# Performance work log

Measured on AMD Instinct MI355X. Metric: run time of the kernel, lower is better.

The kernel has to match this reference:

```python
import jax, jax.numpy as jnp
import numpy as np

N_QUBITS = 8
N_LAYERS = 4
BATCH = 4096


def _ry(theta):
    # RY(theta) = [[cos(t/2), -sin(t/2)], [sin(t/2), cos(t/2)]]
    c = jnp.cos(theta / 2).astype(jnp.complex64)
    s = jnp.sin(theta / 2).astype(jnp.complex64)
    return jnp.stack([jnp.stack([c, -s], axis=-1),
                      jnp.stack([s, c], axis=-1)], axis=-2)  # (..., 2, 2)


def _rz(theta):
    # RZ(theta) = diag(exp(-i t/2), exp(+i t/2))
    p = jnp.exp(-0.5j * theta.astype(jnp.complex64))
    z = jnp.zeros_like(p)
    return jnp.stack([jnp.stack([p, z], axis=-1),
                      jnp.stack([z, jnp.conj(p)], axis=-1)], axis=-2)


def _apply_1q(state, U, w):
    # state: (B, 2, 2, ..., 2); apply 2x2 unitary U on wire w (axis 1+w).
    st = jnp.moveaxis(state, 1 + w, -1)
    if U.ndim == 3:  # per-sample (batched) gate, U: (B, 2, 2)
        st = jnp.einsum('bij,b...j->b...i', U, st)
    else:            # shared gate, U: (2, 2)
        st = jnp.einsum('ij,b...j->b...i', U, st)
    return jnp.moveaxis(st, -1, 1 + w)


def _apply_cnot(state, c, t):
    # flip target wire t where control wire c is |1>
    st = jnp.moveaxis(state, (1 + c, 1 + t), (-2, -1))
    st = jnp.concatenate([st[..., 0:1, :], st[..., 1:2, ::-1]], axis=-2)
    return jnp.moveaxis(st, (-2, -1), (1 + c, 1 + t))


def _circuit(x, weights):
    B = x.shape[0]
    state = jnp.zeros((B,) + (2,) * N_QUBITS, jnp.complex64)
    state = state.at[(slice(None),) + (0,) * N_QUBITS].set(1.0)  # |0...0>
    # Angle encoding: RY(x_i) on each wire, batched over samples
    for i in range(N_QUBITS):
        state = _apply_1q(state, _ry(x[:, i]), i)
    # Variational layers: CNOT ring then RY/RZ rotations
    for l in range(N_LAYERS):
        for i in range(N_QUBITS):
            state = _apply_cnot(state, i, (i + 1) % N_QUBITS)
        for i in range(N_QUBITS):
            state = _apply_1q(state, _ry(weights[l, i, 0]), i)
            state = _apply_1q(state, _rz(weights[l, i, 1]), i)
    # <Z_0> = P(q0=0) - P(q0=1)
    probs = jnp.sum(jnp.abs(state.reshape(B, 2, -1)) ** 2, axis=-1)
    return (probs[:, 0] - probs[:, 1]).astype(jnp.float32)


def setup_inputs() -> dict:
    key = jax.random.key(0)
    k1, k2 = jax.random.split(key)
    x = jax.random.uniform(k1, (BATCH, N_QUBITS), dtype=jnp.float32) * jnp.pi
    weights = jax.random.normal(k2, (N_LAYERS, N_QUBITS, 2), dtype=jnp.float32) * 0.1
    return {"x": x, "weights": weights}


def reference(x, weights):
    return _circuit(x, weights)
```

## Files before the change

kernel.cpp:

```cpp
#include <hip/hip_runtime.h>

#define NQ 8
#define NL 4
#define BATCH 4096


template <int CTRL>
__device__ __forceinline__ float dppx(float v) {
  return __int_as_float(
      __builtin_amdgcn_update_dpp(0, __float_as_int(v), CTRL, 0xF, 0xF, true));
}

__device__ __forceinline__ float swz4(float v) {
  return __int_as_float(
      __builtin_amdgcn_ds_swizzle(__float_as_int(v), 0x101F));
}

template <int W>
__device__ __forceinline__ float xl(float v) {
  if constexpr (W == 0) return dppx<0x128>(v);
  else if constexpr (W == 1) return swz4(v);
  else if constexpr (W == 2) return dppx<0x4E>(v);
  else return dppx<0xB1>(v);
}

template <int W>
__device__ __forceinline__ void ry_gate(float re[16], float im[16],
                                        float c, float s, int lane) {
  if constexpr (W <= 3) {
    const float ss = ((lane >> (3 - W)) & 1) ? s : -s;
#pragma unroll
    for (int r = 0; r < 16; ++r) {
      float pr = xl<W>(re[r]);
      float pi = xl<W>(im[r]);
      re[r] = c * re[r] + ss * pr;
      im[r] = c * im[r] + ss * pi;
    }
  } else {
    constexpr int m = 1 << (7 - W);
#pragma unroll
    for (int r = 0; r < 16; ++r) {
      if ((r & m) == 0) {
        const int r1 = r | m;
        float a0r = re[r], a1r = re[r1];
        float a0i = im[r], a1i = im[r1];
        re[r]  = c * a0r - s * a1r;
        re[r1] = s * a0r + c * a1r;
        im[r]  = c * a0i - s * a1i;
        im[r1] = s * a0i + c * a1i;
      }
    }
  }
}

template <int W>
__device__ __forceinline__ void rz_gate(float re[16], float im[16],
                                        float c, float s, int lane) {
  if constexpr (W <= 3) {
    const float ss = ((lane >> (3 - W)) & 1) ? s : -s;
#pragma unroll
    for (int r = 0; r < 16; ++r) {
      float nr = re[r] * c - im[r] * ss;
      float ni = im[r] * c + re[r] * ss;
      re[r] = nr; im[r] = ni;
    }
  } else {
    constexpr int m = 1 << (7 - W);
#pragma unroll
    for (int r = 0; r < 16; ++r) {
      const float ss = (r & m) ? s : -s;
      float nr = re[r] * c - im[r] * ss;
      float ni = im[r] * c + re[r] * ss;
      re[r] = nr; im[r] = ni;
    }
  }
}

__device__ __forceinline__ void cnot_ring(float re[16], float im[16], int lane) {
  {
    const bool p = (lane & 8) != 0;
#pragma unroll
    for (int r = 0; r < 16; ++r) {
      float pr = swz4(re[r]), pi = swz4(im[r]);
      re[r] = p ? pr : re[r];
      im[r] = p ? pi : im[r];
    }
  }
  {
    const bool p = (lane & 4) != 0;
#pragma unroll
    for (int r = 0; r < 16; ++r) {
      float pr = dppx<0x4E>(re[r]), pi = dppx<0x4E>(im[r]);
      re[r] = p ? pr : re[r];
      im[r] = p ? pi : im[r];
    }
  }
  {
    const bool p = (lane & 2) != 0;
#pragma unroll
    for (int r = 0; r < 16; ++r) {
      float pr = dppx<0xB1>(re[r]), pi = dppx<0xB1>(im[r]);
      re[r] = p ? pr : re[r];
      im[r] = p ? pi : im[r];
    }
  }
  {
    const bool p = (lane & 1) != 0;
#pragma unroll
    for (int r = 0; r < 8; ++r) {
      float t0r = re[r], t1r = re[r + 8];
      re[r] = p ? t1r : t0r; re[r + 8] = p ? t0r : t1r;
      float t0i = im[r], t1i = im[r + 8];
      im[r] = p ? t1i : t0i; im[r + 8] = p ? t0i : t1i;
    }
  }
#pragma unroll
  for (int r = 8; r < 12; ++r) {
    float t = re[r]; re[r] = re[r + 4]; re[r + 4] = t;
    t = im[r]; im[r] = im[r + 4]; im[r + 4] = t;
  }
#pragma unroll
  for (int r = 0; r < 16; ++r) {
    if ((r & 4) && !(r & 2)) {
      float t = re[r]; re[r] = re[r | 2]; re[r | 2] = t;
      t = im[r]; im[r] = im[r | 2]; im[r | 2] = t;
    }
  }
#pragma unroll
  for (int r = 0; r < 16; ++r) {
    if ((r & 2) && !(r & 1)) {
      float t = re[r]; re[r] = re[r | 1]; re[r | 1] = t;
      t = im[r]; im[r] = im[r | 1]; im[r | 1] = t;
    }
  }
#pragma unroll
  for (int r = 1; r < 16; r += 2) {
    re[r] = dppx<0x128>(re[r]);
    im[r] = dppx<0x128>(im[r]);
  }
}

__global__ __launch_bounds__(256) void vqc_kernel(const float* __restrict__ x,
                                                  const float* __restrict__ w,
                                                  float* __restrict__ out) {
  const int lane = (int)(threadIdx.x & 63);
  const int wv = (int)((blockIdx.x * blockDim.x + threadIdx.x) >> 6);
  const int s = wv * 4 + (lane >> 4);

  float re[16], im[16];
#pragma unroll
  for (int r = 0; r < 16; ++r) { re[r] = 0.f; im[r] = 0.f; }
  if ((lane & 15) == 0) re[0] = 1.f;

  {
    const float4 x0 = *(const float4*)&x[s * 8];
    const float4 x1 = *(const float4*)&x[s * 8 + 4];
    float c, sn;
    __sincosf(x0.x * 0.5f, &sn, &c); ry_gate<0>(re, im, c, sn, lane);
    __sincosf(x0.y * 0.5f, &sn, &c); ry_gate<1>(re, im, c, sn, lane);
    __sincosf(x0.z * 0.5f, &sn, &c); ry_gate<2>(re, im, c, sn, lane);
    __sincosf(x0.w * 0.5f, &sn, &c); ry_gate<3>(re, im, c, sn, lane);
    __sincosf(x1.x * 0.5f, &sn, &c); ry_gate<4>(re, im, c, sn, lane);
    __sincosf(x1.y * 0.5f, &sn, &c); ry_gate<5>(re, im, c, sn, lane);
    __sincosf(x1.z * 0.5f, &sn, &c); ry_gate<6>(re, im, c, sn, lane);
    __sincosf(x1.w * 0.5f, &sn, &c); ry_gate<7>(re, im, c, sn, lane);
  }

#pragma unroll
  for (int l = 0; l < NL; ++l) {
    cnot_ring(re, im, lane);
    const float* wl = &w[l * NQ * 2];
#define APPLY_ROT(W) { float cy, sy, cz, sz;            \
    __sincosf(wl[(W) * 2 + 0] * 0.5f, &sy, &cy);        \
    __sincosf(wl[(W) * 2 + 1] * 0.5f, &sz, &cz);        \
    ry_gate<W>(re, im, cy, sy, lane);                   \
    rz_gate<W>(re, im, cz, sz, lane); }
    APPLY_ROT(0) APPLY_ROT(1) APPLY_ROT(2) APPLY_ROT(3)
    APPLY_ROT(4) APPLY_ROT(5) APPLY_ROT(6) APPLY_ROT(7)
#undef APPLY_ROT
  }

  float acc = 0.f;
#pragma unroll
  for (int r = 0; r < 16; ++r) acc += re[r] * re[r] + im[r] * im[r];
  acc = (lane & 8) ? -acc : acc;
  acc += dppx<0xB1>(acc);
  acc += dppx<0x4E>(acc);
  acc += swz4(acc);
  acc += dppx<0x128>(acc);
  if ((lane & 15) == 0) out[s] = acc;
}

extern "C" void kernel_launch(void* const* d_in, const int* in_sizes, int n_in,
                              void* d_out, int out_size, void* d_ws, size_t ws_size,
                              hipStream_t stream) {
  const float* x = (const float*)d_in[0];
  const float* w = (const float*)d_in[1];
  float* out = (float*)d_out;
  (void)in_sizes; (void)n_in; (void)out_size; (void)d_ws; (void)ws_size;

  dim3 grid(BATCH / 16), block(256);
  hipLaunchKernelGGL(vqc_kernel, grid, block, 0, stream, x, w, out);
}
```

Before: 65.39 us.

## Map one sample per wavefront with four amplitudes per lane

Redistributes the 256-amplitude state vector so that each sample occupies a full 64-lane wavefront holding 4 complex amplitudes per lane, instead of 16 lanes holding 16 each. This launches four times as many wavefronts and cuts per-thread register use, exposing more parallelism for a 4096-sample batch. In exchange, more qubits are handled through cross-lane exchanges (DPP, ds_swizzle, and a 32-lane xor shuffle), the final reduction gains extra steps, and every wave repeats the sincos computations.

```diff
diff --git a/kernel.cpp b/kernel.cpp
--- a/kernel.cpp
+++ b/kernel.cpp
@@ -11,63 +11,66 @@
       __builtin_amdgcn_update_dpp(0, __float_as_int(v), CTRL, 0xF, 0xF, true));
 }
 
-__device__ __forceinline__ float swz4(float v) {
+template <int MASK>
+__device__ __forceinline__ float swzx(float v) {
   return __int_as_float(
-      __builtin_amdgcn_ds_swizzle(__float_as_int(v), 0x101F));
+      __builtin_amdgcn_ds_swizzle(__float_as_int(v), (MASK << 10) | 0x1F));
 }
+
+__device__ __forceinline__ float xor32(float v) { return __shfl_xor(v, 32, 64); }
 
 template <int W>
 __device__ __forceinline__ float xl(float v) {
-  if constexpr (W == 0) return dppx<0x128>(v);
-  else if constexpr (W == 1) return swz4(v);
-  else if constexpr (W == 2) return dppx<0x4E>(v);
+  if constexpr (W == 0) return xor32(v);
+  else if constexpr (W == 1) return swzx<16>(v);
+  else if constexpr (W == 2) return dppx<0x128>(v);
+  else if constexpr (W == 3) return swzx<4>(v);
+  else if constexpr (W == 4) return dppx<0x4E>(v);
   else return dppx<0xB1>(v);
 }
 
 template <int W>
-__device__ __forceinline__ void ry_gate(float re[16], float im[16],
+__device__ __forceinline__ void ry_gate(float re[4], float im[4],
                                         float c, float s, int lane) {
-  if constexpr (W <= 3) {
-    const float ss = ((lane >> (3 - W)) & 1) ? s : -s;
+  if constexpr (W <= 5) {
+    const float ss = ((lane >> (5 - W)) & 1) ? s : -s;
+    float pr[4], pi[4];
 #pragma unroll
-    for (int r = 0; r < 16; ++r) {
-      float pr = xl<W>(re[r]);
-      float pi = xl<W>(im[r]);
-      re[r] = c * re[r] + ss * pr;
-      im[r] = c * im[r] + ss * pi;
+    for (int r = 0; r < 4; ++r) { pr[r] = xl<W>(re[r]); pi[r] = xl<W>(im[r]); }
+#pragma unroll
+    for (int r = 0; r < 4; ++r) {
+      re[r] = c * re[r] + ss * pr[r];
+      im[r] = c * im[r] + ss * pi[r];
     }
   } else {
-    constexpr int m = 1 << (7 - W);
+    constexpr int m = (W == 6) ? 2 : 1;
 #pragma unroll
-    for (int r = 0; r < 16; ++r) {
+    for (int r = 0; r < 4; ++r) {
       if ((r & m) == 0) {
         const int r1 = r | m;
-        float a0r = re[r], a1r = re[r1];
-        float a0i = im[r], a1i = im[r1];
-        re[r]  = c * a0r - s * a1r;
-        re[r1] = s * a0r + c * a1r;
-        im[r]  = c * a0i - s * a1i;
-        im[r1] = s * a0i + c * a1i;
+        float a0r = re[r], a1r = re[r1], a0i = im[r], a1i = im[r1];
+        re[r]  = c * a0r - s * a1r;  re[r1] = s * a0r + c * a1r;
+        im[r]  = c * a0i - s * a1i;  im[r1] = s * a0i + c * a1i;
       }
     }
   }
 }
 
 template <int W>
-__device__ __forceinline__ void rz_gate(float re[16], float im[16],
+__device__ __forceinline__ void rz_gate(float re[4], float im[4],
                                         float c, float s, int lane) {
-  if constexpr (W <= 3) {
-    const float ss = ((lane >> (3 - W)) & 1) ? s : -s;
+  if constexpr (W <= 5) {
+    const float ss = ((lane >> (5 - W)) & 1) ? s : -s;
 #pragma unroll
-    for (int r = 0; r < 16; ++r) {
+    for (int r = 0; r < 4; ++r) {
       float nr = re[r] * c - im[r] * ss;
       float ni = im[r] * c + re[r] * ss;
       re[r] = nr; im[r] = ni;
     }
   } else {
-    constexpr int m = 1 << (7 - W);
+    constexpr int m = (W == 6) ? 2 : 1;
 #pragma unroll
-    for (int r = 0; r < 16; ++r) {
+    for (int r = 0; r < 4; ++r) {
       const float ss = (r & m) ? s : -s;
       float nr = re[r] * c - im[r] * ss;
       float ni = im[r] * c + re[r] * ss;
@@ -76,81 +79,50 @@
   }
 }
 
-__device__ __forceinline__ void cnot_ring(float re[16], float im[16], int lane) {
-  {
-    const bool p = (lane & 8) != 0;
+template <int W>
+__device__ __forceinline__ void cnot_lane(float re[4], float im[4], bool p) {
+  float pr[4], pi[4];
 #pragma unroll
-    for (int r = 0; r < 16; ++r) {
-      float pr = swz4(re[r]), pi = swz4(im[r]);
-      re[r] = p ? pr : re[r];
-      im[r] = p ? pi : im[r];
-    }
+  for (int r = 0; r < 4; ++r) { pr[r] = xl<W>(re[r]); pi[r] = xl<W>(im[r]); }
+#pragma unroll
+  for (int r = 0; r < 4; ++r) {
+    re[r] = p ? pr[r] : re[r];
+    im[r] = p ? pi[r] : im[r];
   }
-  {
-    const bool p = (lane & 4) != 0;
-#pragma unroll
-    for (int r = 0; r < 16; ++r) {
-      float pr = dppx<0x4E>(re[r]), pi = dppx<0x4E>(im[r]);
-      re[r] = p ? pr : re[r];
-      im[r] = p ? pi : im[r];
-    }
-  }
-  {
-    const bool p = (lane & 2) != 0;
-#pragma unroll
-    for (int r = 0; r < 16; ++r) {
-      float pr = dppx<0xB1>(re[r]), pi = dppx<0xB1>(im[r]);
-      re[r] = p ? pr : re[r];
-      im[r] = p ? pi : im[r];
-    }
-  }
+}
+
+__device__ __forceinline__ void cnot_ring(float re[4], float im[4], int lane) {
+  cnot_lane<1>(re, im, (lane & 32) != 0);
+  cnot_lane<2>(re, im, (lane & 16) != 0);
+  cnot_lane<3>(re, im, (lane & 8) != 0);
+  cnot_lane<4>(re, im, (lane & 4) != 0);
+  cnot_lane<5>(re, im, (lane & 2) != 0);
   {
     const bool p = (lane & 1) != 0;
 #pragma unroll
-    for (int r = 0; r < 8; ++r) {
-      float t0r = re[r], t1r = re[r + 8];
-      re[r] = p ? t1r : t0r; re[r + 8] = p ? t0r : t1r;
-      float t0i = im[r], t1i = im[r + 8];
-      im[r] = p ? t1i : t0i; im[r + 8] = p ? t0i : t1i;
+    for (int r = 0; r < 2; ++r) {
+      float t0 = re[r], t1 = re[r + 2];
+      re[r] = p ? t1 : t0; re[r + 2] = p ? t0 : t1;
+      t0 = im[r]; t1 = im[r + 2];
+      im[r] = p ? t1 : t0; im[r + 2] = p ? t0 : t1;
     }
   }
-#pragma unroll
-  for (int r = 8; r < 12; ++r) {
-    float t = re[r]; re[r] = re[r + 4]; re[r + 4] = t;
-    t = im[r]; im[r] = im[r + 4]; im[r + 4] = t;
-  }
-#pragma unroll
-  for (int r = 0; r < 16; ++r) {
-    if ((r & 4) && !(r & 2)) {
-      float t = re[r]; re[r] = re[r | 2]; re[r | 2] = t;
-      t = im[r]; im[r] = im[r | 2]; im[r | 2] = t;
-    }
-  }
-#pragma unroll
-  for (int r = 0; r < 16; ++r) {
-    if ((r & 2) && !(r & 1)) {
-      float t = re[r]; re[r] = re[r | 1]; re[r | 1] = t;
-      t = im[r]; im[r] = im[r | 1]; im[r | 1] = t;
-    }
-  }
-#pragma unroll
-  for (int r = 1; r < 16; r += 2) {
-    re[r] = dppx<0x128>(re[r]);
-    im[r] = dppx<0x128>(im[r]);
-  }
+  { float t = re[2]; re[2] = re[3]; re[3] = t;
+    t = im[2]; im[2] = im[3]; im[3] = t; }
+  re[1] = xor32(re[1]); im[1] = xor32(im[1]);
+  re[3] = xor32(re[3]); im[3] = xor32(im[3]);
 }
 
 __global__ __launch_bounds__(256) void vqc_kernel(const float* __restrict__ x,
                                                   const float* __restrict__ w,
                                                   float* __restrict__ out) {
   const int lane = (int)(threadIdx.x & 63);
-  const int wv = (int)((blockIdx.x * blockDim.x + threadIdx.x) >> 6);
-  const int s = wv * 4 + (lane >> 4);
+  const int s = (int)((blockIdx.x * blockDim.x + threadIdx.x) >> 6);
 
-  float re[16], im[16];
+  float re[4], im[4];
 #pragma unroll
-  for (int r = 0; r < 16; ++r) { re[r] = 0.f; im[r] = 0.f; }
-  if ((lane & 15) == 0) re[0] = 1.f;
+  for (int r = 0; r < 4; ++r) { re[r] = 0.f; im[r] = 0.f; }
+  if (lane == 0) re[0] = 1.f;
 
   {
     const float4 x0 = *(const float4*)&x[s * 8];
@@ -182,13 +154,15 @@
 
   float acc = 0.f;
 #pragma unroll
-  for (int r = 0; r < 16; ++r) acc += re[r] * re[r] + im[r] * im[r];
-  acc = (lane & 8) ? -acc : acc;
+  for (int r = 0; r < 4; ++r) acc += re[r] * re[r] + im[r] * im[r];
+  acc = (lane & 32) ? -acc : acc;
   acc += dppx<0xB1>(acc);
   acc += dppx<0x4E>(acc);
-  acc += swz4(acc);
+  acc += swzx<4>(acc);
   acc += dppx<0x128>(acc);
-  if ((lane & 15) == 0) out[s] = acc;
+  acc += swzx<16>(acc);
+  acc += xor32(acc);
+  if (lane == 0) out[s] = acc;
 }
 
 extern "C" void kernel_launch(void* const* d_in, const int* in_sizes, int n_in,
@@ -199,6 +173,6 @@
   float* out = (float*)d_out;
   (void)in_sizes; (void)n_in; (void)out_size; (void)d_ws; (void)ws_size;
 
-  dim3 grid(BATCH / 16), block(256);
+  dim3 grid(BATCH / 4), block(256);
   hipLaunchKernelGGL(vqc_kernel, grid, block, 0, stream, x, w, out);
 }
```

Result: slower. 67.22 us (+2.8%).
